# Optimization experiments

Measured on AMD Instinct MI355X. Metric: run time of the kernel, lower is better.

Reference implementation:

```python
import jax, jax.numpy as jnp
import numpy as np

N_HEAD = 16
MA_K = 0.02          # sigmoid temperature in ma_k_activation
LEAKY_SLOPE = 0.02   # negative_slope in ma_q_activation
NEG_INF = -1e9


def setup_inputs() -> dict:
    key = jax.random.key(0)
    k1, k2, k3, k4 = jax.random.split(key, 4)
    B, T, C = 2, 2048, 1024
    x = jax.random.normal(k1, (B, T, C), dtype=jnp.float32)
    s = 1.0 / np.sqrt(C)
    W_attn = jax.random.normal(k2, (C, 2 * C), dtype=jnp.float32) * s
    W_k2 = jax.random.normal(k3, (C, C), dtype=jnp.float32) * s
    W_proj = jax.random.normal(k4, (C, C), dtype=jnp.float32) * s
    return {"x": x, "W_attn": W_attn, "W_k2": W_k2, "W_proj": W_proj}


def _heads(t, H):
    # [B,T,C] -> [B,H,T,d]
    B, T, C = t.shape
    return t.reshape(B, T, H, C // H).transpose(0, 2, 1, 3)


def reference(x, W_attn, W_k2, W_proj):
    B, T, C = x.shape
    H = N_HEAD
    d = C // H
    scale = 1.0 / jnp.sqrt(jnp.asarray(d, x.dtype))

    qk = x @ W_attn                      # [B,T,2C]
    q, k = jnp.split(qk, 2, axis=-1)
    q = _heads(q, H)                     # [B,H,T,d]
    k = _heads(k, H)
    v = _heads(x, H)                     # v = x

    # --- AR branch: causal softmax attention ---
    scores = jnp.einsum('bhtd,bhsd->bhts', q, k) * scale
    causal = jnp.tril(jnp.ones((T, T), dtype=bool))
    scores = jnp.where(causal, scores, NEG_INF)
    attn = jax.nn.softmax(scores, axis=-1)
    y = jnp.einsum('bhts,bhsd->bhtd', attn, v)   # [B,H,T,d]

    # --- MA branch: causal, softmax-free linear attention on residual ---
    e = v[:, :, 1:, :] - y[:, :, :-1, :]          # [B,H,T-1,d]
    k2 = _heads(x[:, :-1, :] @ W_k2, H)           # [B,H,T-1,d]
    q2 = q[:, :, 1:, :]                           # [B,H,T-1,d]

    qa = -jax.nn.leaky_relu(-q2 * scale, negative_slope=LEAKY_SLOPE)
    ka = jax.nn.sigmoid(MA_K * (k2 * scale))

    w = jnp.einsum('bhtd,bhsd->bhts', qa, ka)     # [B,H,T-1,T-1]
    w = jnp.tril(w)
    y2 = jnp.einsum('bhts,bhsd->bhtd', w, e)      # [B,H,T-1,d]
    y2 = jnp.concatenate([jnp.zeros_like(y2[:, :, :1, :]), y2], axis=2)  # pad front

    def merge(t):  # [B,H,T,d] -> [B,T,C]
        return t.transpose(0, 2, 1, 3).reshape(B, T, C)

    return merge(y) @ W_proj + merge(y2) @ W_proj
```

## Files before the change

kernel.cpp:

```cpp
#include <hip/hip_runtime.h>

typedef unsigned short u16;
typedef u16   u16x4  __attribute__((ext_vector_type(4)));
typedef u16   u16x8  __attribute__((ext_vector_type(8)));
typedef __bf16 bf16x8 __attribute__((ext_vector_type(8)));
typedef float  f32x4  __attribute__((ext_vector_type(4)));

__device__ __forceinline__ float bf2f(u16 v) {
    unsigned u = ((unsigned)v) << 16;
    return __builtin_bit_cast(float, u);
}
__device__ __forceinline__ u16 f2bf(float f) {
    unsigned u = __builtin_bit_cast(unsigned, f);
    u += 0x7fffu + ((u >> 16) & 1u);
    return (u16)(u >> 16);
}

__device__ __forceinline__ void async16(const u16* g, u16* l) {
    __builtin_amdgcn_global_load_lds(
        (const __attribute__((address_space(1))) unsigned int*)g,
        (__attribute__((address_space(3))) unsigned int*)l,
        16, 0, 0);
}

__device__ __forceinline__ size_t kimg_idx(int bh, int s, int d) {
    return ((size_t)(bh * 32 + (s >> 6)) * 4096) + (size_t)(((d >> 3) * 64 + (s & 63)) * 8) + (d & 7);
}
__device__ __forceinline__ size_t vimg_idx(int bh, int s, int d) {
    return ((size_t)(bh * 32 + (s >> 6)) * 4096) + (size_t)((((s & 63) >> 3) * 64 + d) * 8) + (s & 7);
}

__global__ __launch_bounds__(256)
void convert_pack(const float* __restrict__ in, u16* __restrict__ xb,
                  u16* __restrict__ xpack) {
    int i = blockIdx.x * 256 + threadIdx.x;
    int c4 = i & 255, row = i >> 8;
    int s = row & 2047, b = row >> 11;
    float4 v = ((const float4*)in)[i];
    u16x4 o;
    o.x = f2bf(v.x); o.y = f2bf(v.y); o.z = f2bf(v.z); o.w = f2bf(v.w);
    ((u16x4*)xb)[i] = o;
    int h = c4 >> 4, d0 = (c4 & 15) * 4;
    size_t base = vimg_idx(b * 16 + h, s, d0);
    xpack[base]      = o.x;
    xpack[base + 8]  = o.y;
    xpack[base + 16] = o.z;
    xpack[base + 24] = o.w;
}

__global__ __launch_bounds__(256)
void prep_weights(const float* __restrict__ Wa, const float* __restrict__ Wk,
                  const float* __restrict__ Wp, u16* __restrict__ Wta,
                  u16* __restrict__ Wtk, u16* __restrict__ Wtp) {
    __shared__ u16 tile[64][65];
    const int bx = blockIdx.x;
    const float* in; u16* out; int Cd, cx;
    if (bx < 32)      { in = Wa; out = Wta; Cd = 2048; cx = bx; }
    else if (bx < 48) { in = Wk; out = Wtk; Cd = 1024; cx = bx - 32; }
    else              { in = Wp; out = Wtp; Cd = 1024; cx = bx - 48; }
    const int c0 = cx * 64, r0 = blockIdx.y * 64;
    const int tid = threadIdx.x;
#pragma unroll
    for (int i = 0; i < 16; ++i) {
        int idx = tid + i * 256;
        int r = idx >> 6, c = idx & 63;
        tile[r][c] = f2bf(in[(size_t)(r0 + r) * Cd + c0 + c]);
    }
    __syncthreads();
#pragma unroll
    for (int i = 0; i < 16; ++i) {
        int idx = tid + i * 256;
        int r = idx >> 6, c = idx & 63;
        out[(size_t)(c0 + r) * 1024 + r0 + c] = tile[c][r];
    }
}

__global__ __launch_bounds__(256, 3)
void gemm_fused(const u16* __restrict__ A, const u16* __restrict__ Bt,
                u16* __restrict__ qs, u16* __restrict__ kpack,
                u16* __restrict__ kapack) {
    const int K = 1024, NT = K / 32;
    __shared__ __align__(16) u16 As[3][4][128][8];
    __shared__ __align__(16) u16 Bs[3][4][128][8];
    const int tid = threadIdx.x;
    const int wave = tid >> 6, lane = tid & 63;
    const int m0 = blockIdx.y * 128, n0 = blockIdx.x * 128;
    const int wm = (wave >> 1) * 64, wn = (wave & 1) * 64;
    const int q = lane >> 4, mr = lane & 15;

    const int s0 = tid, s1 = 256 + tid;
    const u16* gA0 = A  + (size_t)(m0 + (s0 & 127)) * K + (s0 >> 7) * 8;
    const u16* gA1 = A  + (size_t)(m0 + (s1 & 127)) * K + (s1 >> 7) * 8;
    const u16* gB0 = Bt + (size_t)(n0 + (s0 & 127)) * K + (s0 >> 7) * 8;
    const u16* gB1 = Bt + (size_t)(n0 + (s1 & 127)) * K + (s1 >> 7) * 8;
    u16* const lA = &As[0][0][0][0];
    u16* const lB = &Bs[0][0][0][0];
    const int dA0 = s0 * 8, dA1 = s1 * 8;

    f32x4 acc[4][4];
#pragma unroll
    for (int i = 0; i < 4; ++i)
#pragma unroll
        for (int j = 0; j < 4; ++j) acc[i][j] = f32x4{0.f, 0.f, 0.f, 0.f};

    async16(gA0,      lA + dA0);
    async16(gA1,      lA + dA1);
    async16(gB0,      lB + dA0);
    async16(gB1,      lB + dA1);
    async16(gA0 + 32, lA + 4096 + dA0);
    async16(gA1 + 32, lA + 4096 + dA1);
    async16(gB0 + 32, lB + 4096 + dA0);
    async16(gB1 + 32, lB + 4096 + dA1);

    int co = 0;
    int io = 2 * 4096;
    for (int t = 0; t < NT; ++t) {
        if (t < NT - 1) asm volatile("s_waitcnt vmcnt(4)" ::: "memory");
        else            asm volatile("s_waitcnt vmcnt(0)" ::: "memory");
        __syncthreads();
        if (t + 2 < NT) {
            const int kn = (t + 2) * 32;
            async16(gA0 + kn, lA + io + dA0);
            async16(gA1 + kn, lA + io + dA1);
            async16(gB0 + kn, lB + io + dA0);
            async16(gB1 + kn, lB + io + dA1);
        }
        bf16x8 af[4], bfr[4];
#pragma unroll
        for (int i = 0; i < 4; ++i)
            af[i]  = *(const bf16x8*)(lA + co + (size_t)(q * 128 + wm + i * 16 + mr) * 8);
#pragma unroll
        for (int j = 0; j < 4; ++j)
            bfr[j] = *(const bf16x8*)(lB + co + (size_t)(q * 128 + wn + j * 16 + mr) * 8);
#pragma unroll
        for (int i = 0; i < 4; ++i)
#pragma unroll
            for (int j = 0; j < 4; ++j)
                acc[i][j] = __builtin_amdgcn_mfma_f32_16x16x32_bf16(af[i], bfr[j], acc[i][j], 0, 0, 0);
        co += 4096; if (co == 3 * 4096) co = 0;
        io += 4096; if (io == 3 * 4096) io = 0;
    }
#pragma unroll
    for (int i = 0; i < 4; ++i)
#pragma unroll
        for (int j = 0; j < 4; ++j)
#pragma unroll
            for (int r = 0; r < 4; ++r) {
                int m = m0 + wm + i * 16 + q * 4 + r;
                int n = n0 + wn + j * 16 + mr;
                float v = acc[i][j][r];
                int b = m >> 11, s = m & 2047;
                if (n < 1024) {
                    qs[(size_t)m * 1024 + n] = f2bf(v * 0.125f);
                } else if (n < 2048) {
                    int nn = n - 1024;
                    kpack[kimg_idx(b * 16 + (nn >> 6), s, nn & 63)] = f2bf(v);
                } else {
                    int nn = n - 2048;
                    kapack[kimg_idx(b * 16 + (nn >> 6), s, nn & 63)] =
                        f2bf(1.f / (1.f + __expf(-0.0025f * v)));
                }
            }
}

__global__ __launch_bounds__(256, 2)
void gemm64(const u16* __restrict__ A, const u16* __restrict__ Bt,
            float* __restrict__ Cv, int N, int K) {
    const int NT = K / 32;
    __shared__ __align__(16) u16 As[3][4][64][8];
    __shared__ __align__(16) u16 Bs[3][4][128][8];
    const int tid = threadIdx.x;
    const int wave = tid >> 6, lane = tid & 63;
    const int m0 = blockIdx.y * 64, n0 = blockIdx.x * 128;
    const int wn0 = wave * 32;
    const int q = lane >> 4, mr = lane & 15;

    const u16* gA = A + (size_t)(m0 + (tid & 63)) * K + (tid >> 6) * 8;
    const int s1 = 256 + tid;
    const u16* gB0 = Bt + (size_t)(n0 + (tid & 127)) * K + (tid >> 7) * 8;
    const u16* gB1 = Bt + (size_t)(n0 + (s1 & 127)) * K + (s1 >> 7) * 8;
    u16* const lA = &As[0][0][0][0];
    u16* const lB = &Bs[0][0][0][0];
    const int dA = tid * 8, dB0 = tid * 8, dB1 = s1 * 8;

    f32x4 acc[4][2];
#pragma unroll
    for (int i = 0; i < 4; ++i)
#pragma unroll
        for (int j = 0; j < 2; ++j) acc[i][j] = f32x4{0.f, 0.f, 0.f, 0.f};

    async16(gA,       lA + dA);
    async16(gB0,      lB + dB0);
    async16(gB1,      lB + dB1);
    async16(gA + 32,  lA + 2048 + dA);
    async16(gB0 + 32, lB + 4096 + dB0);
    async16(gB1 + 32, lB + 4096 + dB1);

    int coA = 0, coB = 0, ioA = 2 * 2048, ioB = 2 * 4096;
    for (int t = 0; t < NT; ++t) {
        if (t < NT - 1) asm volatile("s_waitcnt vmcnt(3)" ::: "memory");
        else            asm volatile("s_waitcnt vmcnt(0)" ::: "memory");
        __syncthreads();
        if (t + 2 < NT) {
            const int kn = (t + 2) * 32;
            async16(gA + kn,  lA + ioA + dA);
            async16(gB0 + kn, lB + ioB + dB0);
            async16(gB1 + kn, lB + ioB + dB1);
        }
        bf16x8 af[4], bfr[2];
#pragma unroll
        for (int i = 0; i < 4; ++i)
            af[i]  = *(const bf16x8*)(lA + coA + (size_t)(q * 64 + i * 16 + mr) * 8);
#pragma unroll
        for (int j = 0; j < 2; ++j)
            bfr[j] = *(const bf16x8*)(lB + coB + (size_t)(q * 128 + wn0 + j * 16 + mr) * 8);
#pragma unroll
        for (int i = 0; i < 4; ++i)
#pragma unroll
            for (int j = 0; j < 2; ++j)
                acc[i][j] = __builtin_amdgcn_mfma_f32_16x16x32_bf16(af[i], bfr[j], acc[i][j], 0, 0, 0);
        coA += 2048; if (coA == 3 * 2048) coA = 0;
        coB += 4096; if (coB == 3 * 4096) coB = 0;
        ioA += 2048; if (ioA == 3 * 2048) ioA = 0;
        ioB += 4096; if (ioB == 3 * 4096) ioB = 0;
    }
#pragma unroll
    for (int i = 0; i < 4; ++i)
#pragma unroll
        for (int j = 0; j < 2; ++j)
#pragma unroll
            for (int r = 0; r < 4; ++r) {
                int m = m0 + i * 16 + q * 4 + r;
                int n = n0 + wn0 + j * 16 + mr;
                Cv[(size_t)m * N + n] = acc[i][j][r];
            }
}

__global__ __launch_bounds__(256, 2)
void flash_mfma(const u16* __restrict__ qs, const u16* __restrict__ kpack,
                const u16* __restrict__ xpack, u16* __restrict__ Opart,
                float* __restrict__ lpart) {
    __shared__ __align__(16) u16 Ks[8][64][8];
    __shared__ __align__(16) u16 Vs[8][64][8];
    __shared__ __align__(16) u16 Ps[4][16][72];
    const int bh = blockIdx.y, b = bh >> 4, hc = (bh & 15) * 64;
    const int z = blockIdx.z;
    const int tid = threadIdx.x, w = tid >> 6, lane = tid & 63;
    const int n16 = lane & 15, quad = lane >> 4;
    const u16* kbase = kpack + (size_t)bh * 32 * 4096;
    const u16* vbase = xpack + (size_t)bh * 32 * 4096;
    u16* Ob = Opart + (size_t)z * 4096 * 1024;
    float* lb = lpart + z * 65536;

    for (int rep = 0; rep < 2; ++rep) {
        const int T = rep ? 15 - (int)blockIdx.x : (int)blockIdx.x;
        const int t0 = T * 128;
        const int nchunk = 2 * T + 2;

        bf16x8 qf[2][2];
#pragma unroll
        for (int mt = 0; mt < 2; ++mt) {
            const int trow = t0 + (w + mt * 4) * 16 + n16;
            const u16* qp = &qs[(size_t)(b * 2048 + trow) * 1024 + hc + quad * 8];
            qf[mt][0] = *(const bf16x8*)qp;
            qf[mt][1] = *(const bf16x8*)(qp + 32);
        }

        f32x4 O[2][4];
        float lsum[2][4];
#pragma unroll
        for (int mt = 0; mt < 2; ++mt)
#pragma unroll
            for (int jt = 0; jt < 4; ++jt) { O[mt][jt] = f32x4{0.f, 0.f, 0.f, 0.f}; }
#pragma unroll
        for (int mt = 0; mt < 2; ++mt)
#pragma unroll
            for (int r = 0; r < 4; ++r) lsum[mt][r] = 0.f;

        u16x8 kr0, kr1, vr0, vr1;
        auto pref = [&](int c) {
            const u16* kc = kbase + (size_t)c * 4096;
            const u16* vc = vbase + (size_t)c * 4096;
            kr0 = *(const u16x8*)(kc + tid * 8);
            kr1 = *(const u16x8*)(kc + (256 + tid) * 8);
            vr0 = *(const u16x8*)(vc + tid * 8);
            vr1 = *(const u16x8*)(vc + (256 + tid) * 8);
        };
        if (z < nchunk) pref(z);

        for (int c = z; c < nchunk; c += 2) {
            __syncthreads();
            *(u16x8*)((u16*)Ks + tid * 8)         = kr0;
            *(u16x8*)((u16*)Ks + (256 + tid) * 8) = kr1;
            *(u16x8*)((u16*)Vs + tid * 8)         = vr0;
            *(u16x8*)((u16*)Vs + (256 + tid) * 8) = vr1;
            __syncthreads();
            if (c + 2 < nchunk) pref(c + 2);

            f32x4 S[2][4];
#pragma unroll
            for (int mt = 0; mt < 2; ++mt)
#pragma unroll
                for (int jt = 0; jt < 4; ++jt) S[mt][jt] = f32x4{0.f, 0.f, 0.f, 0.f};
#pragma unroll
            for (int ks = 0; ks < 2; ++ks)
#pragma unroll
                for (int jt = 0; jt < 4; ++jt) {
                    bf16x8 kf = *(const bf16x8*)&Ks[ks * 4 + quad][jt * 16 + n16][0];
                    S[0][jt] = __builtin_amdgcn_mfma_f32_16x16x32_bf16(qf[0][ks], kf, S[0][jt], 0, 0, 0);
                    S[1][jt] = __builtin_amdgcn_mfma_f32_16x16x32_bf16(qf[1][ks], kf, S[1][jt], 0, 0, 0);
                }
            bf16x8 vf[2][4];
#pragma unroll
            for (int ks = 0; ks < 2; ++ks)
#pragma unroll
                for (int jt = 0; jt < 4; ++jt)
                    vf[ks][jt] = *(const bf16x8*)&Vs[ks * 4 + quad][jt * 16 + n16][0];

#pragma unroll
            for (int mt = 0; mt < 2; ++mt) {
                if (mt == 0 && c == 2 * T + 1) continue;
                float p[4][4];
#pragma unroll
                for (int reg = 0; reg < 4; ++reg)
#pragma unroll
                    for (int jt = 0; jt < 4; ++jt)
                        p[reg][jt] = __expf(S[mt][jt][reg]);
                if (c == 2 * T + mt) {
#pragma unroll
                    for (int reg = 0; reg < 4; ++reg) {
                        const int tr = t0 + (w + mt * 4) * 16 + quad * 4 + reg;
#pragma unroll
                        for (int jt = 0; jt < 4; ++jt)
                            if (c * 64 + jt * 16 + n16 > tr) p[reg][jt] = 0.f;
                    }
                }
#pragma unroll
                for (int reg = 0; reg < 4; ++reg) {
                    lsum[mt][reg] += (p[reg][0] + p[reg][1]) + (p[reg][2] + p[reg][3]);
#pragma unroll
                    for (int jt = 0; jt < 4; ++jt)
                        Ps[w][quad * 4 + reg][jt * 16 + n16] = f2bf(p[reg][jt]);
                }
                bf16x8 pf[2];
#pragma unroll
                for (int ks = 0; ks < 2; ++ks)
                    pf[ks] = *(const bf16x8*)&Ps[w][n16][ks * 32 + quad * 8];
#pragma unroll
                for (int ks = 0; ks < 2; ++ks)
#pragma unroll
                    for (int jt = 0; jt < 4; ++jt)
                        O[mt][jt] = __builtin_amdgcn_mfma_f32_16x16x32_bf16(pf[ks], vf[ks][jt], O[mt][jt], 0, 0, 0);
            }
        }

#pragma unroll
        for (int mt = 0; mt < 2; ++mt)
#pragma unroll
            for (int reg = 0; reg < 4; ++reg) {
                float l = lsum[mt][reg];
#pragma unroll
                for (int off = 1; off < 16; off <<= 1) l += __shfl_xor(l, off, 64);
                const int tr = t0 + (w + mt * 4) * 16 + quad * 4 + reg;
                if (n16 == 0) lb[bh * 2048 + tr] = l;
                const size_t row = (size_t)(b * 2048 + tr) * 1024 + hc;
#pragma unroll
                for (int jt = 0; jt < 4; ++jt)
                    Ob[row + jt * 16 + n16] = f2bf(O[mt][jt][reg]);
            }
    }
}

__global__ __launch_bounds__(256)
void combine_flash(const u16* __restrict__ Opart, const float* __restrict__ lpart,
                   const u16* __restrict__ xb, u16* __restrict__ y,
                   u16* __restrict__ epack) {
    int i = blockIdx.x * 256 + threadIdx.x;
    int c4 = i & 255, row = i >> 8, t = row & 2047, b = row >> 11;
    int h = c4 >> 4, d0 = (c4 & 15) * 4;
    size_t off = (size_t)row * 1024 + c4 * 4;
    u16x4 o0 = *(const u16x4*)&Opart[off];
    u16x4 o1 = *(const u16x4*)&Opart[(size_t)4096 * 1024 + off];
    int lrow = (b * 16 + h) * 2048 + t;
    float inv = 1.f / (lpart[lrow] + lpart[65536 + lrow]);
    float y0 = (bf2f(o0.x) + bf2f(o1.x)) * inv;
    float y1 = (bf2f(o0.y) + bf2f(o1.y)) * inv;
    float y2 = (bf2f(o0.z) + bf2f(o1.z)) * inv;
    float y3 = (bf2f(o0.w) + bf2f(o1.w)) * inv;
    u16x4 yo;
    yo.x = f2bf(y0); yo.y = f2bf(y1); yo.z = f2bf(y2); yo.w = f2bf(y3);
    *(u16x4*)&y[off] = yo;
    float e0 = 0.f, e1 = 0.f, e2 = 0.f, e3 = 0.f;
    if (t < 2047) {
        u16x4 xv = *(const u16x4*)&xb[off + 1024];
        e0 = bf2f(xv.x) - y0; e1 = bf2f(xv.y) - y1;
        e2 = bf2f(xv.z) - y2; e3 = bf2f(xv.w) - y3;
    }
    size_t base = vimg_idx(b * 16 + h, t, d0);
    epack[base]      = f2bf(e0);
    epack[base + 8]  = f2bf(e1);
    epack[base + 16] = f2bf(e2);
    epack[base + 24] = f2bf(e3);
}

__global__ __launch_bounds__(256, 2)
void arma_mfma(const u16* __restrict__ qs, const u16* __restrict__ kapack,
               const u16* __restrict__ epack, u16* __restrict__ Opart) {
    __shared__ __align__(16) u16 Ks[8][64][8];
    __shared__ __align__(16) u16 Es[8][64][8];
    __shared__ __align__(16) u16 Ps[4][16][72];
    const int bh = blockIdx.y, b = bh >> 4, hc = (bh & 15) * 64;
    const int z = blockIdx.z;
    const int tid = threadIdx.x, w = tid >> 6, lane = tid & 63;
    const int n16 = lane & 15, quad = lane >> 4;
    const u16* kbase = kapack + (size_t)bh * 32 * 4096;
    const u16* vbase = epack + (size_t)bh * 32 * 4096;
    u16* Ob = Opart + (size_t)z * 4096 * 1024;

    for (int rep = 0; rep < 2; ++rep) {
        const int T = rep ? 15 - (int)blockIdx.x : (int)blockIdx.x;
        const int t0 = T * 128;
        const int nchunk = 2 * T + 2;

        bf16x8 qf[2][2];
#pragma unroll
        for (int mt = 0; mt < 2; ++mt) {
            const int trow = t0 + (w + mt * 4) * 16 + n16;
            const u16* qp = &qs[(size_t)(b * 2048 + trow) * 1024 + hc + quad * 8];
#pragma unroll
            for (int ks = 0; ks < 2; ++ks) {
                u16x8 qv = *(const u16x8*)(qp + ks * 32);
                u16x8 o;
#pragma unroll
                for (int j = 0; j < 8; ++j) {
                    float zv = bf2f(qv[j]);
                    o[j] = f2bf(zv < 0.f ? zv : 0.02f * zv);
                }
                qf[mt][ks] = __builtin_bit_cast(bf16x8, o);
            }
        }

        f32x4 O[2][4];
#pragma unroll
        for (int mt = 0; mt < 2; ++mt)
#pragma unroll
            for (int jt = 0; jt < 4; ++jt) O[mt][jt] = f32x4{0.f, 0.f, 0.f, 0.f};

        u16x8 kr0, kr1, vr0, vr1;
        auto pref = [&](int c) {
            const u16* kc = kbase + (size_t)c * 4096;
            const u16* vc = vbase + (size_t)c * 4096;
            kr0 = *(const u16x8*)(kc + tid * 8);
            kr1 = *(const u16x8*)(kc + (256 + tid) * 8);
            vr0 = *(const u16x8*)(vc + tid * 8);
            vr1 = *(const u16x8*)(vc + (256 + tid) * 8);
        };
        if (z < nchunk) pref(z);

        for (int c = z; c < nchunk; c += 2) {
            __syncthreads();
            *(u16x8*)((u16*)Ks + tid * 8)         = kr0;
            *(u16x8*)((u16*)Ks + (256 + tid) * 8) = kr1;
            *(u16x8*)((u16*)Es + tid * 8)         = vr0;
            *(u16x8*)((u16*)Es + (256 + tid) * 8) = vr1;
            __syncthreads();
            if (c + 2 < nchunk) pref(c + 2);

            f32x4 S[2][4];
#pragma unroll
            for (int mt = 0; mt < 2; ++mt)
#pragma unroll
                for (int jt = 0; jt < 4; ++jt) S[mt][jt] = f32x4{0.f, 0.f, 0.f, 0.f};
#pragma unroll
            for (int ks = 0; ks < 2; ++ks)
#pragma unroll
                for (int jt = 0; jt < 4; ++jt) {
                    bf16x8 kf = *(const bf16x8*)&Ks[ks * 4 + quad][jt * 16 + n16][0];
                    S[0][jt] = __builtin_amdgcn_mfma_f32_16x16x32_bf16(qf[0][ks], kf, S[0][jt], 0, 0, 0);
                    S[1][jt] = __builtin_amdgcn_mfma_f32_16x16x32_bf16(qf[1][ks], kf, S[1][jt], 0, 0, 0);
                }
            bf16x8 vf[2][4];
#pragma unroll
            for (int ks = 0; ks < 2; ++ks)
#pragma unroll
                for (int jt = 0; jt < 4; ++jt)
                    vf[ks][jt] = *(const bf16x8*)&Es[ks * 4 + quad][jt * 16 + n16][0];

#pragma unroll
            for (int mt = 0; mt < 2; ++mt) {
                if (mt == 0 && c == 2 * T + 1) continue;
                if (c == 2 * T + mt) {
#pragma unroll
                    for (int reg = 0; reg < 4; ++reg) {
                        const int tr = t0 + (w + mt * 4) * 16 + quad * 4 + reg;
#pragma unroll
                        for (int jt = 0; jt < 4; ++jt)
                            if (c * 64 + jt * 16 + n16 >= tr) S[mt][jt][reg] = 0.f;
                    }
                }
#pragma unroll
                for (int reg = 0; reg < 4; ++reg)
#pragma unroll
                    for (int jt = 0; jt < 4; ++jt)
                        Ps[w][quad * 4 + reg][jt * 16 + n16] = f2bf(S[mt][jt][reg]);
                bf16x8 pf[2];
#pragma unroll
                for (int ks = 0; ks < 2; ++ks)
                    pf[ks] = *(const bf16x8*)&Ps[w][n16][ks * 32 + quad * 8];
#pragma unroll
                for (int ks = 0; ks < 2; ++ks)
#pragma unroll
                    for (int jt = 0; jt < 4; ++jt)
                        O[mt][jt] = __builtin_amdgcn_mfma_f32_16x16x32_bf16(pf[ks], vf[ks][jt], O[mt][jt], 0, 0, 0);
            }
        }

#pragma unroll
        for (int mt = 0; mt < 2; ++mt)
#pragma unroll
            for (int reg = 0; reg < 4; ++reg) {
                const int tr = t0 + (w + mt * 4) * 16 + quad * 4 + reg;
                const size_t row = (size_t)(b * 2048 + tr) * 1024 + hc;
#pragma unroll
                for (int jt = 0; jt < 4; ++jt)
                    Ob[row + jt * 16 + n16] = f2bf(O[mt][jt][reg]);
            }
    }
}

__global__ __launch_bounds__(256)
void combine_arma(const u16* __restrict__ Opart, const u16* __restrict__ y,
                  u16* __restrict__ ys) {
    int i = blockIdx.x * 256 + threadIdx.x;
    size_t off = (size_t)i * 4;
    u16x4 o0 = *(const u16x4*)&Opart[off];
    u16x4 o1 = *(const u16x4*)&Opart[(size_t)4096 * 1024 + off];
    u16x4 yv = *(const u16x4*)&y[off];
    u16x4 r;
    r.x = f2bf(bf2f(yv.x) + bf2f(o0.x) + bf2f(o1.x));
    r.y = f2bf(bf2f(yv.y) + bf2f(o0.y) + bf2f(o1.y));
    r.z = f2bf(bf2f(yv.z) + bf2f(o0.z) + bf2f(o1.z));
    r.w = f2bf(bf2f(yv.w) + bf2f(o0.w) + bf2f(o1.w));
    *(u16x4*)&ys[off] = r;
}

extern "C" void kernel_launch(void* const* d_in, const int* in_sizes, int n_in,
                              void* d_out, int out_size, void* d_ws, size_t ws_size,
                              hipStream_t stream) {
    const float* x      = (const float*)d_in[0];
    const float* W_attn = (const float*)d_in[1];
    const float* W_k2   = (const float*)d_in[2];
    const float* W_proj = (const float*)d_in[3];
    float* out = (float*)d_out;

    char* w = (char*)d_ws;
    u16* xb      = (u16*)w; w += (size_t)4096 * 1024 * 2;
    u16* Wt_attn = (u16*)w; w += (size_t)2048 * 1024 * 2;
    u16* Wt_k2   = (u16*)w; w += (size_t)1024 * 1024 * 2;
    u16* Wt_proj = (u16*)w; w += (size_t)1024 * 1024 * 2;
    u16* qs      = (u16*)w; w += (size_t)4096 * 1024 * 2;
    u16* kpack   = (u16*)w; w += (size_t)4096 * 1024 * 2;
    u16* kapack  = (u16*)w; w += (size_t)4096 * 1024 * 2;
    u16* xpack   = (u16*)w; w += (size_t)4096 * 1024 * 2;
    u16* y       = (u16*)w; w += (size_t)4096 * 1024 * 2;
    u16* epack   = (u16*)w; w += (size_t)4096 * 1024 * 2;
    u16* Opart   = (u16*)w; w += (size_t)2 * 4096 * 1024 * 2;
    float* lpart = (float*)w; w += (size_t)2 * 65536 * 4;
    u16* ys = xb;

    convert_pack<<<dim3(4096), dim3(256), 0, stream>>>(x, xb, xpack);
    prep_weights<<<dim3(64, 16), dim3(256), 0, stream>>>(W_attn, W_k2, W_proj,
                                                         Wt_attn, Wt_k2, Wt_proj);
    gemm_fused<<<dim3(24, 32), dim3(256), 0, stream>>>(xb, Wt_attn, qs, kpack, kapack);
    flash_mfma<<<dim3(8, 32, 2), dim3(256), 0, stream>>>(qs, kpack, xpack, Opart, lpart);
    combine_flash<<<dim3(4096), dim3(256), 0, stream>>>(Opart, lpart, xb, y, epack);
    arma_mfma<<<dim3(8, 32, 2), dim3(256), 0, stream>>>(qs, kapack, epack, Opart);
    combine_arma<<<dim3(4096), dim3(256), 0, stream>>>(Opart, y, ys);
    gemm64<<<dim3(8, 64), dim3(256), 0, stream>>>(ys, Wt_proj, out, 1024, 1024);
}
```

Measured before the change: 294.9 us.

## Pre-pack GEMM operands into tile-contiguous images for coalesced async LDS loads

The producer kernels (convert_pack, prep_weights, combine_arma) now write GEMM operands directly in the per-tile, per-k-step LDS image layout, so each 32-wide k slice of a 128- or 64-row tile is one contiguous 8 KB or 4 KB block. The GEMM kernels then issue fully contiguous 16-byte async loads instead of strided row reads, which should improve global load coalescing and cut address arithmetic. The cost is scattered stores in the producers, and the A image for gemm_fused reuses the Opart buffer before flash_mfma overwrites it.

New measurement: 268.6 us. -8.9%, faster.

```diff
diff --git a/kernel.cpp b/kernel.cpp
--- a/kernel.cpp
+++ b/kernel.cpp
@@ -30,9 +30,18 @@
     return ((size_t)(bh * 32 + (s >> 6)) * 4096) + (size_t)((((s & 63) >> 3) * 64 + d) * 8) + (s & 7);
 }
 
+__device__ __forceinline__ size_t g128_idx(int m, int k) {
+    return ((size_t)((m >> 7) * 32 + (k >> 5)) * 4096)
+         + (size_t)((((k >> 3) & 3) * 128 + (m & 127)) * 8 + (k & 7));
+}
+__device__ __forceinline__ size_t g64_idx(int m, int k) {
+    return ((size_t)((m >> 6) * 32 + (k >> 5)) * 2048)
+         + (size_t)((((k >> 3) & 3) * 64 + (m & 63)) * 8 + (k & 7));
+}
+
 __global__ __launch_bounds__(256)
 void convert_pack(const float* __restrict__ in, u16* __restrict__ xb,
-                  u16* __restrict__ xpack) {
+                  u16* __restrict__ xpack, u16* __restrict__ agimg) {
     int i = blockIdx.x * 256 + threadIdx.x;
     int c4 = i & 255, row = i >> 8;
     int s = row & 2047, b = row >> 11;
@@ -46,19 +55,21 @@
     xpack[base + 8]  = o.y;
     xpack[base + 16] = o.z;
     xpack[base + 24] = o.w;
+    int k0 = c4 * 4;
+    *(u16x4*)&agimg[g128_idx(row, k0)] = o;
 }
 
 __global__ __launch_bounds__(256)
 void prep_weights(const float* __restrict__ Wa, const float* __restrict__ Wk,
-                  const float* __restrict__ Wp, u16* __restrict__ Wta,
-                  u16* __restrict__ Wtk, u16* __restrict__ Wtp) {
+                  const float* __restrict__ Wp, u16* __restrict__ bgimg,
+                  u16* __restrict__ bpimg) {
     __shared__ u16 tile[64][65];
     const int bx = blockIdx.x;
-    const float* in; u16* out; int Cd, cx;
-    if (bx < 32)      { in = Wa; out = Wta; Cd = 2048; cx = bx; }
-    else if (bx < 48) { in = Wk; out = Wtk; Cd = 1024; cx = bx - 32; }
-    else              { in = Wp; out = Wtp; Cd = 1024; cx = bx - 48; }
-    const int c0 = cx * 64, r0 = blockIdx.y * 64;
+    const float* in; u16* img; int Cd, c0, nbase;
+    if (bx < 32)      { in = Wa; img = bgimg; Cd = 2048; c0 = bx * 64;        nbase = c0; }
+    else if (bx < 48) { in = Wk; img = bgimg; Cd = 1024; c0 = (bx - 32) * 64; nbase = 2048 + c0; }
+    else              { in = Wp; img = bpimg; Cd = 1024; c0 = (bx - 48) * 64; nbase = c0; }
+    const int r0 = blockIdx.y * 64;
     const int tid = threadIdx.x;
 #pragma unroll
     for (int i = 0; i < 16; ++i) {
@@ -71,15 +82,16 @@
     for (int i = 0; i < 16; ++i) {
         int idx = tid + i * 256;
         int r = idx >> 6, c = idx & 63;
-        out[(size_t)(c0 + r) * 1024 + r0 + c] = tile[c][r];
+        int n = nbase + r, k = r0 + c;
+        img[g128_idx(n, k)] = tile[c][r];
     }
 }
 
 __global__ __launch_bounds__(256, 3)
-void gemm_fused(const u16* __restrict__ A, const u16* __restrict__ Bt,
+void gemm_fused(const u16* __restrict__ Aimg, const u16* __restrict__ Bimg,
                 u16* __restrict__ qs, u16* __restrict__ kpack,
                 u16* __restrict__ kapack) {
-    const int K = 1024, NT = K / 32;
+    const int NT = 32;
     __shared__ __align__(16) u16 As[3][4][128][8];
     __shared__ __align__(16) u16 Bs[3][4][128][8];
     const int tid = threadIdx.x;
@@ -88,14 +100,11 @@
     const int wm = (wave >> 1) * 64, wn = (wave & 1) * 64;
     const int q = lane >> 4, mr = lane & 15;
 
-    const int s0 = tid, s1 = 256 + tid;
-    const u16* gA0 = A  + (size_t)(m0 + (s0 & 127)) * K + (s0 >> 7) * 8;
-    const u16* gA1 = A  + (size_t)(m0 + (s1 & 127)) * K + (s1 >> 7) * 8;
-    const u16* gB0 = Bt + (size_t)(n0 + (s0 & 127)) * K + (s0 >> 7) * 8;
-    const u16* gB1 = Bt + (size_t)(n0 + (s1 & 127)) * K + (s1 >> 7) * 8;
+    const u16* gA = Aimg + (size_t)blockIdx.y * 32 * 4096;
+    const u16* gB = Bimg + (size_t)blockIdx.x * 32 * 4096;
     u16* const lA = &As[0][0][0][0];
     u16* const lB = &Bs[0][0][0][0];
-    const int dA0 = s0 * 8, dA1 = s1 * 8;
+    const int d0 = tid * 8, d1 = (256 + tid) * 8;
 
     f32x4 acc[4][4];
 #pragma unroll
@@ -103,14 +112,14 @@
 #pragma unroll
         for (int j = 0; j < 4; ++j) acc[i][j] = f32x4{0.f, 0.f, 0.f, 0.f};
 
-    async16(gA0,      lA + dA0);
-    async16(gA1,      lA + dA1);
-    async16(gB0,      lB + dA0);
-    async16(gB1,      lB + dA1);
-    async16(gA0 + 32, lA + 4096 + dA0);
-    async16(gA1 + 32, lA + 4096 + dA1);
-    async16(gB0 + 32, lB + 4096 + dA0);
-    async16(gB1 + 32, lB + 4096 + dA1);
+    async16(gA + d0,        lA + d0);
+    async16(gA + d1,        lA + d1);
+    async16(gB + d0,        lB + d0);
+    async16(gB + d1,        lB + d1);
+    async16(gA + 4096 + d0, lA + 4096 + d0);
+    async16(gA + 4096 + d1, lA + 4096 + d1);
+    async16(gB + 4096 + d0, lB + 4096 + d0);
+    async16(gB + 4096 + d1, lB + 4096 + d1);
 
     int co = 0;
     int io = 2 * 4096;
@@ -119,11 +128,11 @@
         else            asm volatile("s_waitcnt vmcnt(0)" ::: "memory");
         __syncthreads();
         if (t + 2 < NT) {
-            const int kn = (t + 2) * 32;
-            async16(gA0 + kn, lA + io + dA0);
-            async16(gA1 + kn, lA + io + dA1);
-            async16(gB0 + kn, lB + io + dA0);
-            async16(gB1 + kn, lB + io + dA1);
+            const int sg = (t + 2) * 4096;
+            async16(gA + sg + d0, lA + io + d0);
+            async16(gA + sg + d1, lA + io + d1);
+            async16(gB + sg + d0, lB + io + d0);
+            async16(gB + sg + d1, lB + io + d1);
         }
         bf16x8 af[4], bfr[4];
 #pragma unroll
@@ -164,9 +173,9 @@
 }
 
 __global__ __launch_bounds__(256, 2)
-void gemm64(const u16* __restrict__ A, const u16* __restrict__ Bt,
+void gemm64(const u16* __restrict__ Aimg, const u16* __restrict__ Bimg,
             float* __restrict__ Cv, int N, int K) {
-    const int NT = K / 32;
+    const int NT = 32;
     __shared__ __align__(16) u16 As[3][4][64][8];
     __shared__ __align__(16) u16 Bs[3][4][128][8];
     const int tid = threadIdx.x;
@@ -175,13 +184,11 @@
     const int wn0 = wave * 32;
     const int q = lane >> 4, mr = lane & 15;
 
-    const u16* gA = A + (size_t)(m0 + (tid & 63)) * K + (tid >> 6) * 8;
-    const int s1 = 256 + tid;
-    const u16* gB0 = Bt + (size_t)(n0 + (tid & 127)) * K + (tid >> 7) * 8;
-    const u16* gB1 = Bt + (size_t)(n0 + (s1 & 127)) * K + (s1 >> 7) * 8;
+    const u16* gA = Aimg + (size_t)blockIdx.y * 32 * 2048;
+    const u16* gB = Bimg + (size_t)blockIdx.x * 32 * 4096;
     u16* const lA = &As[0][0][0][0];
     u16* const lB = &Bs[0][0][0][0];
-    const int dA = tid * 8, dB0 = tid * 8, dB1 = s1 * 8;
+    const int d0 = tid * 8, d1 = (256 + tid) * 8;
 
     f32x4 acc[4][2];
 #pragma unroll
@@ -189,12 +196,12 @@
 #pragma unroll
         for (int j = 0; j < 2; ++j) acc[i][j] = f32x4{0.f, 0.f, 0.f, 0.f};
 
-    async16(gA,       lA + dA);
-    async16(gB0,      lB + dB0);
-    async16(gB1,      lB + dB1);
-    async16(gA + 32,  lA + 2048 + dA);
-    async16(gB0 + 32, lB + 4096 + dB0);
-    async16(gB1 + 32, lB + 4096 + dB1);
+    async16(gA + d0,        lA + d0);
+    async16(gB + d0,        lB + d0);
+    async16(gB + d1,        lB + d1);
+    async16(gA + 2048 + d0, lA + 2048 + d0);
+    async16(gB + 4096 + d0, lB + 4096 + d0);
+    async16(gB + 4096 + d1, lB + 4096 + d1);
 
     int coA = 0, coB = 0, ioA = 2 * 2048, ioB = 2 * 4096;
     for (int t = 0; t < NT; ++t) {
@@ -202,10 +209,9 @@
         else            asm volatile("s_waitcnt vmcnt(0)" ::: "memory");
         __syncthreads();
         if (t + 2 < NT) {
-            const int kn = (t + 2) * 32;
-            async16(gA + kn,  lA + ioA + dA);
-            async16(gB0 + kn, lB + ioB + dB0);
-            async16(gB1 + kn, lB + ioB + dB1);
+            async16(gA + (t + 2) * 2048 + d0, lA + ioA + d0);
+            async16(gB + (t + 2) * 4096 + d0, lB + ioB + d0);
+            async16(gB + (t + 2) * 4096 + d1, lB + ioB + d1);
         }
         bf16x8 af[4], bfr[2];
 #pragma unroll
@@ -530,9 +536,10 @@
 
 __global__ __launch_bounds__(256)
 void combine_arma(const u16* __restrict__ Opart, const u16* __restrict__ y,
-                  u16* __restrict__ ys) {
+                  u16* __restrict__ ysimg) {
     int i = blockIdx.x * 256 + threadIdx.x;
     size_t off = (size_t)i * 4;
+    int row = i >> 8, col = (i & 255) * 4;
     u16x4 o0 = *(const u16x4*)&Opart[off];
     u16x4 o1 = *(const u16x4*)&Opart[(size_t)4096 * 1024 + off];
     u16x4 yv = *(const u16x4*)&y[off];
@@ -541,7 +548,7 @@
     r.y = f2bf(bf2f(yv.y) + bf2f(o0.y) + bf2f(o1.y));
     r.z = f2bf(bf2f(yv.z) + bf2f(o0.z) + bf2f(o1.z));
     r.w = f2bf(bf2f(yv.w) + bf2f(o0.w) + bf2f(o1.w));
-    *(u16x4*)&ys[off] = r;
+    *(u16x4*)&ysimg[g64_idx(row, col)] = r;
 }
 
 extern "C" void kernel_launch(void* const* d_in, const int* in_sizes, int n_in,
@@ -555,9 +562,8 @@
 
     char* w = (char*)d_ws;
     u16* xb      = (u16*)w; w += (size_t)4096 * 1024 * 2;
-    u16* Wt_attn = (u16*)w; w += (size_t)2048 * 1024 * 2;
-    u16* Wt_k2   = (u16*)w; w += (size_t)1024 * 1024 * 2;
-    u16* Wt_proj = (u16*)w; w += (size_t)1024 * 1024 * 2;
+    u16* bgimg   = (u16*)w; w += (size_t)3072 * 1024 * 2;
+    u16* bpimg   = (u16*)w; w += (size_t)1024 * 1024 * 2;
     u16* qs      = (u16*)w; w += (size_t)4096 * 1024 * 2;
     u16* kpack   = (u16*)w; w += (size_t)4096 * 1024 * 2;
     u16* kapack  = (u16*)w; w += (size_t)4096 * 1024 * 2;
@@ -566,15 +572,16 @@
     u16* epack   = (u16*)w; w += (size_t)4096 * 1024 * 2;
     u16* Opart   = (u16*)w; w += (size_t)2 * 4096 * 1024 * 2;
     float* lpart = (float*)w; w += (size_t)2 * 65536 * 4;
-    u16* ys = xb;
-
-    convert_pack<<<dim3(4096), dim3(256), 0, stream>>>(x, xb, xpack);
+    u16* agimg = Opart;
+    u16* ysimg = xb;
+
+    convert_pack<<<dim3(4096), dim3(256), 0, stream>>>(x, xb, xpack, agimg);
     prep_weights<<<dim3(64, 16), dim3(256), 0, stream>>>(W_attn, W_k2, W_proj,
-                                                         Wt_attn, Wt_k2, Wt_proj);
-    gemm_fused<<<dim3(24, 32), dim3(256), 0, stream>>>(xb, Wt_attn, qs, kpack, kapack);
+                                                         bgimg, bpimg);
+    gemm_fused<<<dim3(24, 32), dim3(256), 0, stream>>>(agimg, bgimg, qs, kpack, kapack);
     flash_mfma<<<dim3(8, 32, 2), dim3(256), 0, stream>>>(qs, kpack, xpack, Opart, lpart);
     combine_flash<<<dim3(4096), dim3(256), 0, stream>>>(Opart, lpart, xb, y, epack);
     arma_mfma<<<dim3(8, 32, 2), dim3(256), 0, stream>>>(qs, kapack, epack, Opart);
-    combine_arma<<<dim3(4096), dim3(256), 0, stream>>>(Opart, y, ys);
-    gemm64<<<dim3(8, 64), dim3(256), 0, stream>>>(ys, Wt_proj, out, 1024, 1024);
-}
+    combine_arma<<<dim3(4096), dim3(256), 0, stream>>>(Opart, y, ysimg);
+    gemm64<<<dim3(8, 64), dim3(256), 0, stream>>>(ysimg, bpimg, out, 1024, 1024);
+}
```
